# Kernel tuning notes

Hardware: AMD Instinct MI355X
Metric: run time of the kernel (lower is better)

## Reference

```python
import jax, jax.numpy as jnp
import numpy as np

N_NODES = 50000


def sage_conv(x, src, dst, W_l, b_l, W_r, n_nodes):
    """PyG SAGEConv with mean aggregation: lin_l(mean_{j->i} x_j) + lin_r(x_i)."""
    msg = x[src]                                            # [E, d]
    agg = jax.ops.segment_sum(msg, dst, num_segments=n_nodes)
    cnt = jax.ops.segment_sum(jnp.ones((src.shape[0],), x.dtype), dst,
                              num_segments=n_nodes)
    agg = agg / jnp.maximum(cnt, 1.0)[:, None]              # mean over in-neighbors
    return agg @ W_l.T + b_l + x @ W_r.T


def setup_inputs() -> dict:
    key = jax.random.key(0)
    ks = jax.random.split(key, 8)
    d_in, d_hid, d_out = 128, 128, 64
    E = 600000
    x = jax.random.normal(ks[0], (N_NODES, d_in), dtype=jnp.float32)
    edge_index = jax.random.randint(ks[1], (2, E), 0, N_NODES, dtype=jnp.int64)
    s = 1.0 / np.sqrt(d_in)
    return {
        "x": x,
        "edge_index": edge_index,
        "W1_l": jax.random.normal(ks[2], (d_hid, d_in), jnp.float32) * s,
        "b1": jnp.zeros((d_hid,), jnp.float32),
        "W1_r": jax.random.normal(ks[3], (d_hid, d_in), jnp.float32) * s,
        "W2_l": jax.random.normal(ks[4], (d_out, d_hid), jnp.float32) * s,
        "b2": jnp.zeros((d_out,), jnp.float32),
        "W2_r": jax.random.normal(ks[5], (d_out, d_hid), jnp.float32) * s,
    }


def reference(x, edge_index, W1_l, b1, W1_r, W2_l, b2, W2_r):
    src, dst = edge_index[0], edge_index[1]
    h = sage_conv(x, src, dst, W1_l, b1, W1_r, N_NODES)
    h = jax.nn.relu(h)
    h = sage_conv(h, src, dst, W2_l, b2, W2_r, N_NODES)
    return jax.nn.log_softmax(h, axis=1)
```

## Files before the change

kernel.cpp:

```cpp
#include <hip/hip_runtime.h>
#include <math.h>

#define N_NODES 50000
#define D 128
#define D_OUT 64

typedef short bf16x8 __attribute__((ext_vector_type(8)));
typedef float f32x4  __attribute__((ext_vector_type(4)));
typedef unsigned short u16x8 __attribute__((ext_vector_type(8)));

__device__ __forceinline__ unsigned short f_to_bf16(float f) {
    unsigned int u = __float_as_uint(f);
    u = (u + 0x7fffu + ((u >> 16) & 1u)) >> 16;
    return (unsigned short)u;
}
__device__ __forceinline__ float bf16lo(unsigned int v) { return __uint_as_float(v << 16); }
__device__ __forceinline__ float bf16hi(unsigned int v) { return __uint_as_float(v & 0xffff0000u); }
__device__ __forceinline__ float bf16f(unsigned short v) { return __uint_as_float((unsigned int)v << 16); }

__device__ __forceinline__ void conv8(const float* __restrict__ src, unsigned short* __restrict__ dst, int i)
{
    float4 v0 = *reinterpret_cast<const float4*>(src + i);
    float4 v1 = *reinterpret_cast<const float4*>(src + i + 4);
    u16x8 o;
    o[0] = f_to_bf16(v0.x); o[1] = f_to_bf16(v0.y);
    o[2] = f_to_bf16(v0.z); o[3] = f_to_bf16(v0.w);
    o[4] = f_to_bf16(v1.x); o[5] = f_to_bf16(v1.y);
    o[6] = f_to_bf16(v1.z); o[7] = f_to_bf16(v1.w);
    *reinterpret_cast<u16x8*>(dst + i) = o;
}

__device__ __forceinline__ void acc_add(float* acc, uint4 v)
{
    acc[0] += bf16lo(v.x); acc[1] += bf16hi(v.x);
    acc[2] += bf16lo(v.y); acc[3] += bf16hi(v.y);
    acc[4] += bf16lo(v.z); acc[5] += bf16hi(v.z);
    acc[6] += bf16lo(v.w); acc[7] += bf16hi(v.w);
}

__global__ __launch_bounds__(256) void zero_kernel(int* __restrict__ p, int n4)
{
    int i = blockIdx.x * 256 + threadIdx.x;
    if (i < n4) *reinterpret_cast<int4*>(p + i * 4) = make_int4(0, 0, 0, 0);
}

__global__ __launch_bounds__(256) void prep_kernel(
    const float* __restrict__ x, unsigned short* __restrict__ xb,
    const float* __restrict__ w1l, const float* __restrict__ w1r,
    const float* __restrict__ w2l, const float* __restrict__ w2r,
    unsigned short* __restrict__ Wb,
    const int* __restrict__ dst, int* __restrict__ deg,
    int XB, int E)
{
    const int bx = blockIdx.x;
    if (bx < XB) {
        int i = (bx * 256 + threadIdx.x) * 8;
        if (i < N_NODES * D) conv8(x, xb, i);
    } else if (bx < XB + 24) {
        int i = ((bx - XB) * 256 + threadIdx.x) * 8;
        const float* src; int off;
        if      (i < 16384) { src = w1l; off = 0; }
        else if (i < 32768) { src = w1r; off = 16384; }
        else if (i < 40960) { src = w2l; off = 32768; }
        else                { src = w2r; off = 40960; }
        conv8(src, Wb + off, i - off);
    } else {
        int e = (bx - XB - 24) * 256 + threadIdx.x;
        if (e < E) atomicAdd(&deg[dst[e]], 1);
    }
}

__global__ __launch_bounds__(256) void scan1_kernel(
    const int* __restrict__ deg, int* __restrict__ part,
    int* __restrict__ bsum, int n)
{
    const int t = threadIdx.x;
    const int base = blockIdx.x * 1024 + t * 4;

    int a0 = 0, a1 = 0, a2 = 0, a3 = 0;
    if (base + 3 < n) {
        int4 v = *reinterpret_cast<const int4*>(deg + base);
        a0 = v.x; a1 = v.y; a2 = v.z; a3 = v.w;
    } else if (base < n) {
        a0 = deg[base];
        if (base + 1 < n) a1 = deg[base + 1];
        if (base + 2 < n) a2 = deg[base + 2];
    }
    const int s0 = a0, s1 = s0 + a1, s2 = s1 + a2, s3 = s2 + a3;

    const int lane = t & 63;
    int incl = s3;
#pragma unroll
    for (int off = 1; off < 64; off <<= 1) {
        int up = __shfl_up(incl, off);
        if (lane >= off) incl += up;
    }

    __shared__ int wsum[4];
    const int wid = t >> 6;
    if (lane == 63) wsum[wid] = incl;
    __syncthreads();

    int woff = 0;
#pragma unroll
    for (int w = 0; w < 4; ++w) woff += (w < wid) ? wsum[w] : 0;

    const int ex = woff + incl - s3;
    if (base + 3 < n) {
        int4 o; o.x = ex; o.y = ex + s0; o.z = ex + s1; o.w = ex + s2;
        *reinterpret_cast<int4*>(part + base) = o;
    } else if (base < n) {
        part[base] = ex;
        if (base + 1 < n) part[base + 1] = ex + s0;
        if (base + 2 < n) part[base + 2] = ex + s1;
    }
    if (t == 255) bsum[blockIdx.x] = woff + incl;
}

__global__ __launch_bounds__(64) void scan2_kernel(
    int* __restrict__ bsum, int* __restrict__ row_ptr, int nb, int n)
{
    const int t = threadIdx.x;
    int v = (t < nb) ? bsum[t] : 0;
    int incl = v;
#pragma unroll
    for (int off = 1; off < 64; off <<= 1) {
        int up = __shfl_up(incl, off);
        if (t >= off) incl += up;
    }
    if (t < nb) bsum[t] = incl - v;
    if (t == 63) row_ptr[n] = incl;
}

__global__ __launch_bounds__(256) void scan3_kernel(
    const int* __restrict__ part, const int* __restrict__ bsum,
    int* __restrict__ row_ptr, int n)
{
    const int base = blockIdx.x * 1024 + threadIdx.x * 4;
    const int add = bsum[blockIdx.x];
    if (base + 3 < n) {
        int4 v = *reinterpret_cast<const int4*>(part + base);
        v.x += add; v.y += add; v.z += add; v.w += add;
        *reinterpret_cast<int4*>(row_ptr + base) = v;
    } else if (base < n) {
        row_ptr[base] = part[base] + add;
        if (base + 1 < n) row_ptr[base + 1] = part[base + 1] + add;
        if (base + 2 < n) row_ptr[base + 2] = part[base + 2] + add;
    }
}

__global__ __launch_bounds__(256) void fill_kernel(
    const int* __restrict__ src, const int* __restrict__ dst,
    const int* __restrict__ row_ptr, int* __restrict__ cursor,
    int* __restrict__ esrc, int E)
{
    int e = blockIdx.x * blockDim.x + threadIdx.x;
    if (e >= E) return;
    int d = dst[e];
    int pos = atomicAdd(&cursor[d], 1);
    esrc[row_ptr[d] + pos] = src[e];
}

template<int CHUNKS>
__global__ __launch_bounds__(256) void gather_bf16_kernel(
    const unsigned short* __restrict__ xb,
    const int* __restrict__ row_ptr,
    const int* __restrict__ esrc,
    unsigned short* __restrict__ aggb,
    int n_nodes)
{
    constexpr int RPL = 64 / CHUNKS;
    constexpr int NLOADS = 16 / RPL;
    const int wv   = threadIdx.x >> 6;
    const int lane = threadIdx.x & 63;
    const int node = blockIdx.x * 4 + wv;
    if (node >= n_nodes) return;

    const int beg = row_ptr[node];
    const int end = row_ptr[node + 1];
    const int g = lane / CHUNKS;
    const int c = lane % CHUNKS;

    const uint4* x4 = reinterpret_cast<const uint4*>(xb);

    float acc[8];
#pragma unroll
    for (int k = 0; k < 8; ++k) acc[k] = 0.f;

    for (int base = beg; base < end; base += 64) {
        const int cnt = min(end - base, 64);
        int s = (base + lane < end) ? esrc[base + lane] : 0;
        for (int i = 0; i < cnt; i += 16) {
            int pp[NLOADS];
            uint4 vv[NLOADS];
#pragma unroll
            for (int j = 0; j < NLOADS; ++j) {
                pp[j] = i + j * RPL + g;
                int sj = __shfl(s, pp[j]);
                vv[j] = x4[(size_t)sj * CHUNKS + c];
            }
#pragma unroll
            for (int j = 0; j < NLOADS; ++j)
                if (pp[j] < cnt) acc_add(acc, vv[j]);
        }
    }

#pragma unroll
    for (int k = 0; k < 8; ++k) {
#pragma unroll
        for (int off = CHUNKS; off < 64; off <<= 1)
            acc[k] += __shfl_xor(acc[k], off);
    }

    if (g == 0) {
        const float inv = (end > beg) ? 1.0f / (float)(end - beg) : 0.0f;
        uint4 o;
        o.x = (unsigned int)f_to_bf16(acc[0] * inv) | ((unsigned int)f_to_bf16(acc[1] * inv) << 16);
        o.y = (unsigned int)f_to_bf16(acc[2] * inv) | ((unsigned int)f_to_bf16(acc[3] * inv) << 16);
        o.z = (unsigned int)f_to_bf16(acc[4] * inv) | ((unsigned int)f_to_bf16(acc[5] * inv) << 16);
        o.w = (unsigned int)f_to_bf16(acc[6] * inv) | ((unsigned int)f_to_bf16(acc[7] * inv) << 16);
        reinterpret_cast<uint4*>(aggb)[(size_t)node * CHUNKS + c] = o;
    }
}

__global__ __launch_bounds__(64) void layer1_mfma_kernel(
    const unsigned short* __restrict__ aggb,
    const unsigned short* __restrict__ xb,
    const unsigned short* __restrict__ Wb,
    const float* __restrict__ b1,
    unsigned short* __restrict__ h1b,
    unsigned short* __restrict__ t2b)
{
    __shared__ unsigned short h1s[16][144];

    const int lane  = threadIdx.x;
    const int node0 = blockIdx.x * 16;
    const int c16   = lane & 15;
    const int kg    = lane >> 4;

    bf16x8 a[2][4];
    {
        const unsigned short* A0 = aggb + (size_t)(node0 + c16) * D + kg * 8;
        const unsigned short* A1 = xb   + (size_t)(node0 + c16) * D + kg * 8;
#pragma unroll
        for (int kf = 0; kf < 4; ++kf) {
            a[0][kf] = *reinterpret_cast<const bf16x8*>(A0 + kf * 32);
            a[1][kf] = *reinterpret_cast<const bf16x8*>(A1 + kf * 32);
        }
    }
    const unsigned short* WL = Wb;
    const unsigned short* WR = Wb + 16384;

#pragma unroll 2
    for (int jt = 0; jt < 8; ++jt) {
        f32x4 acc = {0.f, 0.f, 0.f, 0.f};
        const unsigned short* wl = WL + (size_t)(jt * 16 + c16) * D + kg * 8;
        const unsigned short* wr = WR + (size_t)(jt * 16 + c16) * D + kg * 8;
#pragma unroll
        for (int kf = 0; kf < 4; ++kf) {
            bf16x8 b = *reinterpret_cast<const bf16x8*>(wl + kf * 32);
            acc = __builtin_amdgcn_mfma_f32_16x16x32_bf16(a[0][kf], b, acc, 0, 0, 0);
        }
#pragma unroll
        for (int kf = 0; kf < 4; ++kf) {
            bf16x8 b = *reinterpret_cast<const bf16x8*>(wr + kf * 32);
            acc = __builtin_amdgcn_mfma_f32_16x16x32_bf16(a[1][kf], b, acc, 0, 0, 0);
        }
        const float bias = b1[jt * 16 + c16];
#pragma unroll
        for (int i = 0; i < 4; ++i) {
            float v = fmaxf(acc[i] + bias, 0.0f);
            unsigned short us = f_to_bf16(v);
            h1b[(size_t)(node0 + kg * 4 + i) * D + jt * 16 + c16] = us;
            h1s[kg * 4 + i][jt * 16 + c16] = us;
        }
    }

    __syncthreads();

    bf16x8 a2[4];
#pragma unroll
    for (int kf = 0; kf < 4; ++kf)
        a2[kf] = *reinterpret_cast<const bf16x8*>(&h1s[c16][kg * 8 + kf * 32]);

    const unsigned short* W2L = Wb + 32768;
#pragma unroll
    for (int jt = 0; jt < 4; ++jt) {
        f32x4 acc = {0.f, 0.f, 0.f, 0.f};
        const unsigned short* wl = W2L + (size_t)(jt * 16 + c16) * D + kg * 8;
#pragma unroll
        for (int kf = 0; kf < 4; ++kf) {
            bf16x8 b = *reinterpret_cast<const bf16x8*>(wl + kf * 32);
            acc = __builtin_amdgcn_mfma_f32_16x16x32_bf16(a2[kf], b, acc, 0, 0, 0);
        }
#pragma unroll
        for (int i = 0; i < 4; ++i)
            t2b[(size_t)(node0 + kg * 4 + i) * D_OUT + jt * 16 + c16] = f_to_bf16(acc[i]);
    }
}

__global__ __launch_bounds__(64) void layer2_mfma_kernel(
    const unsigned short* __restrict__ agg2b,
    const unsigned short* __restrict__ h1b,
    const unsigned short* __restrict__ Wb,
    const float* __restrict__ b2,
    float* __restrict__ out)
{
    const int lane  = threadIdx.x;
    const int node0 = blockIdx.x * 16;
    const int c16   = lane & 15;
    const int kg    = lane >> 4;

    bf16x8 a[4];
    {
        const unsigned short* A1 = h1b + (size_t)(node0 + c16) * D + kg * 8;
#pragma unroll
        for (int kf = 0; kf < 4; ++kf)
            a[kf] = *reinterpret_cast<const bf16x8*>(A1 + kf * 32);
    }
    const unsigned short* WR = Wb + 40960;

    f32x4 accs[4];
#pragma unroll
    for (int jt = 0; jt < 4; ++jt) {
        f32x4 acc = {0.f, 0.f, 0.f, 0.f};
        const unsigned short* wr = WR + (size_t)(jt * 16 + c16) * D + kg * 8;
#pragma unroll
        for (int kf = 0; kf < 4; ++kf) {
            bf16x8 b = *reinterpret_cast<const bf16x8*>(wr + kf * 32);
            acc = __builtin_amdgcn_mfma_f32_16x16x32_bf16(a[kf], b, acc, 0, 0, 0);
        }
        accs[jt] = acc;
    }

    float bias[4];
#pragma unroll
    for (int jt = 0; jt < 4; ++jt) bias[jt] = b2[jt * 16 + c16];

#pragma unroll
    for (int i = 0; i < 4; ++i) {
        const int node = node0 + kg * 4 + i;
        float z[4];
        float m = -1e30f;
#pragma unroll
        for (int jt = 0; jt < 4; ++jt) {
            float lft = bf16f(agg2b[(size_t)node * D_OUT + jt * 16 + c16]);
            z[jt] = lft + accs[jt][i] + bias[jt];
            m = fmaxf(m, z[jt]);
        }
#pragma unroll
        for (int off = 1; off < 16; off <<= 1)
            m = fmaxf(m, __shfl_xor(m, off));
        float s = 0.f;
#pragma unroll
        for (int jt = 0; jt < 4; ++jt) s += expf(z[jt] - m);
#pragma unroll
        for (int off = 1; off < 16; off <<= 1)
            s += __shfl_xor(s, off);
        float lse = m + logf(s);
#pragma unroll
        for (int jt = 0; jt < 4; ++jt)
            out[(size_t)node * D_OUT + jt * 16 + c16] = z[jt] - lse;
    }
}

extern "C" void kernel_launch(void* const* d_in, const int* in_sizes, int n_in,
                              void* d_out, int out_size, void* d_ws, size_t ws_size,
                              hipStream_t stream)
{
    const float* x   = (const float*)d_in[0];
    const int*   ei  = (const int*)d_in[1];
    const float* W1l = (const float*)d_in[2];
    const float* b1  = (const float*)d_in[3];
    const float* W1r = (const float*)d_in[4];
    const float* W2l = (const float*)d_in[5];
    const float* b2  = (const float*)d_in[6];
    const float* W2r = (const float*)d_in[7];
    float* out = (float*)d_out;

    const int E = in_sizes[1] / 2;
    const int* src = ei;
    const int* dst = ei + E;

    char* base = (char*)d_ws;
    size_t off = 0;
    auto take = [&](size_t bytes) { char* p = base + off; off += (bytes + 255) & ~(size_t)255; return p; };

    unsigned short* xb    = (unsigned short*)take((size_t)N_NODES * D * 2);
    unsigned short* aggb  = (unsigned short*)take((size_t)N_NODES * D * 2);
    unsigned short* h1b   = (unsigned short*)take((size_t)N_NODES * D * 2);
    unsigned short* t2b   = (unsigned short*)take((size_t)N_NODES * D_OUT * 2);
    unsigned short* agg2b = (unsigned short*)take((size_t)N_NODES * D_OUT * 2);
    unsigned short* Wb    = (unsigned short*)take((size_t)49152 * 2);
    int* degcur  = (int*)take((size_t)2 * N_NODES * 4);
    int* deg     = degcur;
    int* cursor  = degcur + N_NODES;
    int* row_ptr = (int*)take(((size_t)N_NODES + 1) * 4);
    int* part    = (int*)take((size_t)N_NODES * 4);
    int* bsum    = (int*)take((size_t)64 * 4);
    int* esrc    = (int*)take((size_t)E * 4);

    const int EB = (E + 255) / 256;
    const int SB = (N_NODES + 1023) / 1024;
    const int XB = (N_NODES * D / 8 + 255) / 256;

    zero_kernel<<<(2 * N_NODES / 4 + 255) / 256, 256, 0, stream>>>(degcur, 2 * N_NODES / 4);
    prep_kernel<<<XB + 24 + EB, 256, 0, stream>>>(x, xb, W1l, W1r, W2l, W2r, Wb, dst, deg, XB, E);
    scan1_kernel<<<SB, 256, 0, stream>>>(deg, part, bsum, N_NODES);
    scan2_kernel<<<1, 64, 0, stream>>>(bsum, row_ptr, SB, N_NODES);
    scan3_kernel<<<SB, 256, 0, stream>>>(part, bsum, row_ptr, N_NODES);
    fill_kernel<<<EB, 256, 0, stream>>>(src, dst, row_ptr, cursor, esrc, E);

    const int GB = (N_NODES + 3) / 4;
    const int MB = N_NODES / 16;

    gather_bf16_kernel<16><<<GB, 256, 0, stream>>>(xb, row_ptr, esrc, aggb, N_NODES);
    layer1_mfma_kernel<<<MB, 64, 0, stream>>>(aggb, xb, Wb, b1, h1b, t2b);

    gather_bf16_kernel<8><<<GB, 256, 0, stream>>>(t2b, row_ptr, esrc, agg2b, N_NODES);
    layer2_mfma_kernel<<<MB, 64, 0, stream>>>(agg2b, h1b, Wb, b2, out);
}
```

Baseline: 167.1 us.

## Fuse CSR build into persistent kernel and fuse gathers with MFMA layers

The degree count, three-stage scan and fill are merged into one persistent 512-block kernel that uses software grid barriers. Each gather is fused with its dense MFMA layer, so the aggregated rows stay in shared memory instead of round-tripping through global buffers. The launch count drops from ten to four. Risks: the grid barrier can deadlock if not all 512 blocks are co-resident, and the fused gather kernels run with fewer waves per node block, which may reduce memory-level parallelism during the gathers.

New measurement: 285.2 us. +70.6%, slower.

```diff
diff --git a/kernel.cpp b/kernel.cpp
--- a/kernel.cpp
+++ b/kernel.cpp
@@ -4,6 +4,7 @@
 #define N_NODES 50000
 #define D 128
 #define D_OUT 64
+#define CSRB 512
 
 typedef short bf16x8 __attribute__((ext_vector_type(8)));
 typedef float f32x4  __attribute__((ext_vector_type(4)));
@@ -38,19 +39,13 @@
     acc[6] += bf16lo(v.w); acc[7] += bf16hi(v.w);
 }
 
-__global__ __launch_bounds__(256) void zero_kernel(int* __restrict__ p, int n4)
-{
-    int i = blockIdx.x * 256 + threadIdx.x;
-    if (i < n4) *reinterpret_cast<int4*>(p + i * 4) = make_int4(0, 0, 0, 0);
-}
-
-__global__ __launch_bounds__(256) void prep_kernel(
+__global__ __launch_bounds__(256) void conv_kernel(
     const float* __restrict__ x, unsigned short* __restrict__ xb,
     const float* __restrict__ w1l, const float* __restrict__ w1r,
     const float* __restrict__ w2l, const float* __restrict__ w2r,
     unsigned short* __restrict__ Wb,
-    const int* __restrict__ dst, int* __restrict__ deg,
-    int XB, int E)
+    int* __restrict__ degcur, int* __restrict__ bar,
+    int XB, int ZB)
 {
     const int bx = blockIdx.x;
     if (bx < XB) {
@@ -64,207 +59,200 @@
         else if (i < 40960) { src = w2l; off = 32768; }
         else                { src = w2r; off = 40960; }
         conv8(src, Wb + off, i - off);
+    } else if (bx < XB + 24 + ZB) {
+        int i = (bx - XB - 24) * 256 + threadIdx.x;
+        if (i < 2 * N_NODES / 4)
+            *reinterpret_cast<int4*>(degcur + i * 4) = make_int4(0, 0, 0, 0);
     } else {
-        int e = (bx - XB - 24) * 256 + threadIdx.x;
-        if (e < E) atomicAdd(&deg[dst[e]], 1);
-    }
-}
-
-__global__ __launch_bounds__(256) void scan1_kernel(
-    const int* __restrict__ deg, int* __restrict__ part,
-    int* __restrict__ bsum, int n)
-{
+        if (threadIdx.x < 16) bar[threadIdx.x] = 0;
+    }
+}
+
+__device__ __forceinline__ void gbar(int* bar, int idx, int nblk)
+{
+    __syncthreads();
+    if (threadIdx.x == 0) {
+        __threadfence();
+        __hip_atomic_fetch_add(&bar[idx], 1, __ATOMIC_ACQ_REL, __HIP_MEMORY_SCOPE_AGENT);
+        while (__hip_atomic_load(&bar[idx], __ATOMIC_ACQUIRE, __HIP_MEMORY_SCOPE_AGENT) < nblk)
+            __builtin_amdgcn_s_sleep(1);
+        __threadfence();
+    }
+    __syncthreads();
+}
+
+__global__ __launch_bounds__(256, 2) void csr_kernel(
+    const int* __restrict__ src, const int* __restrict__ dst,
+    int* __restrict__ deg, int* __restrict__ cursor,
+    int* __restrict__ row_ptr, int* __restrict__ part,
+    int* __restrict__ bsum, int* __restrict__ esrc,
+    int* __restrict__ bar, int E)
+{
+    __shared__ int wsum[4];
+    __shared__ int sAdd, sTot;
     const int t = threadIdx.x;
-    const int base = blockIdx.x * 1024 + t * 4;
-
-    int a0 = 0, a1 = 0, a2 = 0, a3 = 0;
-    if (base + 3 < n) {
-        int4 v = *reinterpret_cast<const int4*>(deg + base);
-        a0 = v.x; a1 = v.y; a2 = v.z; a3 = v.w;
-    } else if (base < n) {
-        a0 = deg[base];
-        if (base + 1 < n) a1 = deg[base + 1];
-        if (base + 2 < n) a2 = deg[base + 2];
-    }
-    const int s0 = a0, s1 = s0 + a1, s2 = s1 + a2, s3 = s2 + a3;
-
-    const int lane = t & 63;
-    int incl = s3;
-#pragma unroll
-    for (int off = 1; off < 64; off <<= 1) {
-        int up = __shfl_up(incl, off);
-        if (lane >= off) incl += up;
-    }
-
-    __shared__ int wsum[4];
-    const int wid = t >> 6;
-    if (lane == 63) wsum[wid] = incl;
-    __syncthreads();
-
-    int woff = 0;
-#pragma unroll
-    for (int w = 0; w < 4; ++w) woff += (w < wid) ? wsum[w] : 0;
-
-    const int ex = woff + incl - s3;
-    if (base + 3 < n) {
-        int4 o; o.x = ex; o.y = ex + s0; o.z = ex + s1; o.w = ex + s2;
-        *reinterpret_cast<int4*>(part + base) = o;
-    } else if (base < n) {
-        part[base] = ex;
-        if (base + 1 < n) part[base + 1] = ex + s0;
-        if (base + 2 < n) part[base + 2] = ex + s1;
-    }
-    if (t == 255) bsum[blockIdx.x] = woff + incl;
-}
-
-__global__ __launch_bounds__(64) void scan2_kernel(
-    int* __restrict__ bsum, int* __restrict__ row_ptr, int nb, int n)
-{
-    const int t = threadIdx.x;
-    int v = (t < nb) ? bsum[t] : 0;
-    int incl = v;
-#pragma unroll
-    for (int off = 1; off < 64; off <<= 1) {
-        int up = __shfl_up(incl, off);
-        if (t >= off) incl += up;
-    }
-    if (t < nb) bsum[t] = incl - v;
-    if (t == 63) row_ptr[n] = incl;
-}
-
-__global__ __launch_bounds__(256) void scan3_kernel(
-    const int* __restrict__ part, const int* __restrict__ bsum,
-    int* __restrict__ row_ptr, int n)
-{
-    const int base = blockIdx.x * 1024 + threadIdx.x * 4;
-    const int add = bsum[blockIdx.x];
-    if (base + 3 < n) {
-        int4 v = *reinterpret_cast<const int4*>(part + base);
-        v.x += add; v.y += add; v.z += add; v.w += add;
-        *reinterpret_cast<int4*>(row_ptr + base) = v;
-    } else if (base < n) {
-        row_ptr[base] = part[base] + add;
-        if (base + 1 < n) row_ptr[base + 1] = part[base + 1] + add;
-        if (base + 2 < n) row_ptr[base + 2] = part[base + 2] + add;
-    }
-}
-
-__global__ __launch_bounds__(256) void fill_kernel(
-    const int* __restrict__ src, const int* __restrict__ dst,
-    const int* __restrict__ row_ptr, int* __restrict__ cursor,
-    int* __restrict__ esrc, int E)
-{
-    int e = blockIdx.x * blockDim.x + threadIdx.x;
-    if (e >= E) return;
-    int d = dst[e];
-    int pos = atomicAdd(&cursor[d], 1);
-    esrc[row_ptr[d] + pos] = src[e];
-}
-
-template<int CHUNKS>
-__global__ __launch_bounds__(256) void gather_bf16_kernel(
+    const int bid = blockIdx.x;
+
+    for (int e = bid * 256 + t; e < E; e += CSRB * 256)
+        atomicAdd(&deg[dst[e]], 1);
+    gbar(bar, 0, CSRB);
+
+    if (bid < 49) {
+        const int base = bid * 1024 + t * 4;
+        int a0 = 0, a1 = 0, a2 = 0, a3 = 0;
+        if (base + 3 < N_NODES) {
+            int4 v = *reinterpret_cast<const int4*>(deg + base);
+            a0 = v.x; a1 = v.y; a2 = v.z; a3 = v.w;
+        } else if (base < N_NODES) {
+            a0 = deg[base];
+            if (base + 1 < N_NODES) a1 = deg[base + 1];
+            if (base + 2 < N_NODES) a2 = deg[base + 2];
+        }
+        const int s0 = a0, s1 = s0 + a1, s2 = s1 + a2, s3 = s2 + a3;
+
+        const int lane = t & 63;
+        int incl = s3;
+#pragma unroll
+        for (int off = 1; off < 64; off <<= 1) {
+            int up = __shfl_up(incl, off);
+            if (lane >= off) incl += up;
+        }
+        const int wid = t >> 6;
+        if (lane == 63) wsum[wid] = incl;
+        __syncthreads();
+        int woff = 0;
+#pragma unroll
+        for (int w = 0; w < 4; ++w) woff += (w < wid) ? wsum[w] : 0;
+
+        const int ex = woff + incl - s3;
+        if (base + 3 < N_NODES) {
+            int4 o; o.x = ex; o.y = ex + s0; o.z = ex + s1; o.w = ex + s2;
+            *reinterpret_cast<int4*>(part + base) = o;
+        } else if (base < N_NODES) {
+            part[base] = ex;
+            if (base + 1 < N_NODES) part[base + 1] = ex + s0;
+            if (base + 2 < N_NODES) part[base + 2] = ex + s1;
+        }
+        if (t == 255) bsum[bid] = woff + incl;
+    }
+    gbar(bar, 1, CSRB);
+
+    if (bid < 49) {
+        if (t < 64) {
+            int v   = (t < 49) ? bsum[t] : 0;
+            int pre = (t < bid) ? v : 0;
+            int add = pre, tot = v;
+#pragma unroll
+            for (int off = 1; off < 64; off <<= 1) {
+                add += __shfl_xor(add, off);
+                tot += __shfl_xor(tot, off);
+            }
+            if (t == 0) { sAdd = add; sTot = tot; }
+        }
+        __syncthreads();
+        const int add = sAdd;
+        const int base = bid * 1024 + t * 4;
+        if (base + 3 < N_NODES) {
+            int4 v = *reinterpret_cast<const int4*>(part + base);
+            v.x += add; v.y += add; v.z += add; v.w += add;
+            *reinterpret_cast<int4*>(row_ptr + base) = v;
+        } else if (base < N_NODES) {
+            row_ptr[base] = part[base] + add;
+            if (base + 1 < N_NODES) row_ptr[base + 1] = part[base + 1] + add;
+            if (base + 2 < N_NODES) row_ptr[base + 2] = part[base + 2] + add;
+        }
+        if (bid == 48 && t == 0) row_ptr[N_NODES] = sTot;
+    }
+    gbar(bar, 2, CSRB);
+
+    for (int e = bid * 256 + t; e < E; e += CSRB * 256) {
+        int d = dst[e];
+        int pos = atomicAdd(&cursor[d], 1);
+        esrc[row_ptr[d] + pos] = src[e];
+    }
+}
+
+__global__ __launch_bounds__(256) void gather_layer1_kernel(
     const unsigned short* __restrict__ xb,
-    const int* __restrict__ row_ptr,
-    const int* __restrict__ esrc,
-    unsigned short* __restrict__ aggb,
-    int n_nodes)
-{
-    constexpr int RPL = 64 / CHUNKS;
-    constexpr int NLOADS = 16 / RPL;
-    const int wv   = threadIdx.x >> 6;
-    const int lane = threadIdx.x & 63;
-    const int node = blockIdx.x * 4 + wv;
-    if (node >= n_nodes) return;
-
-    const int beg = row_ptr[node];
-    const int end = row_ptr[node + 1];
-    const int g = lane / CHUNKS;
-    const int c = lane % CHUNKS;
-
-    const uint4* x4 = reinterpret_cast<const uint4*>(xb);
-
-    float acc[8];
-#pragma unroll
-    for (int k = 0; k < 8; ++k) acc[k] = 0.f;
-
-    for (int base = beg; base < end; base += 64) {
-        const int cnt = min(end - base, 64);
-        int s = (base + lane < end) ? esrc[base + lane] : 0;
-        for (int i = 0; i < cnt; i += 16) {
-            int pp[NLOADS];
-            uint4 vv[NLOADS];
-#pragma unroll
-            for (int j = 0; j < NLOADS; ++j) {
-                pp[j] = i + j * RPL + g;
-                int sj = __shfl(s, pp[j]);
-                vv[j] = x4[(size_t)sj * CHUNKS + c];
-            }
-#pragma unroll
-            for (int j = 0; j < NLOADS; ++j)
-                if (pp[j] < cnt) acc_add(acc, vv[j]);
-        }
-    }
-
-#pragma unroll
-    for (int k = 0; k < 8; ++k) {
-#pragma unroll
-        for (int off = CHUNKS; off < 64; off <<= 1)
-            acc[k] += __shfl_xor(acc[k], off);
-    }
-
-    if (g == 0) {
-        const float inv = (end > beg) ? 1.0f / (float)(end - beg) : 0.0f;
-        uint4 o;
-        o.x = (unsigned int)f_to_bf16(acc[0] * inv) | ((unsigned int)f_to_bf16(acc[1] * inv) << 16);
-        o.y = (unsigned int)f_to_bf16(acc[2] * inv) | ((unsigned int)f_to_bf16(acc[3] * inv) << 16);
-        o.z = (unsigned int)f_to_bf16(acc[4] * inv) | ((unsigned int)f_to_bf16(acc[5] * inv) << 16);
-        o.w = (unsigned int)f_to_bf16(acc[6] * inv) | ((unsigned int)f_to_bf16(acc[7] * inv) << 16);
-        reinterpret_cast<uint4*>(aggb)[(size_t)node * CHUNKS + c] = o;
-    }
-}
-
-__global__ __launch_bounds__(64) void layer1_mfma_kernel(
-    const unsigned short* __restrict__ aggb,
-    const unsigned short* __restrict__ xb,
+    const int* __restrict__ row_ptr, const int* __restrict__ esrc,
     const unsigned short* __restrict__ Wb,
     const float* __restrict__ b1,
-    unsigned short* __restrict__ h1b,
-    unsigned short* __restrict__ t2b)
-{
-    __shared__ unsigned short h1s[16][144];
-
-    const int lane  = threadIdx.x;
+    unsigned short* __restrict__ h1b, unsigned short* __restrict__ t2b)
+{
+    __shared__ unsigned short aggs[16][136];
+    __shared__ unsigned short h1s[16][136];
+
+    const int t = threadIdx.x;
+    const int wv = t >> 6, lane = t & 63;
     const int node0 = blockIdx.x * 16;
-    const int c16   = lane & 15;
-    const int kg    = lane >> 4;
-
-    bf16x8 a[2][4];
-    {
-        const unsigned short* A0 = aggb + (size_t)(node0 + c16) * D + kg * 8;
-        const unsigned short* A1 = xb   + (size_t)(node0 + c16) * D + kg * 8;
-#pragma unroll
-        for (int kf = 0; kf < 4; ++kf) {
-            a[0][kf] = *reinterpret_cast<const bf16x8*>(A0 + kf * 32);
-            a[1][kf] = *reinterpret_cast<const bf16x8*>(A1 + kf * 32);
-        }
-    }
-    const unsigned short* WL = Wb;
-    const unsigned short* WR = Wb + 16384;
-
-#pragma unroll 2
-    for (int jt = 0; jt < 8; ++jt) {
+    const int g = lane >> 4, c = lane & 15;
+    const uint4* x4 = reinterpret_cast<const uint4*>(xb);
+
+    for (int i4 = 0; i4 < 4; ++i4) {
+        const int ln = wv * 4 + i4;
+        const int node = node0 + ln;
+        const int beg = row_ptr[node], end = row_ptr[node + 1];
+
+        float acc[8];
+#pragma unroll
+        for (int k = 0; k < 8; ++k) acc[k] = 0.f;
+
+        for (int base = beg; base < end; base += 64) {
+            const int cnt = min(end - base, 64);
+            int s = (base + lane < end) ? esrc[base + lane] : 0;
+            for (int i = 0; i < cnt; i += 16) {
+                int pp[4]; uint4 vv[4];
+#pragma unroll
+                for (int j = 0; j < 4; ++j) {
+                    pp[j] = i + j * 4 + g;
+                    int sj = __shfl(s, pp[j]);
+                    vv[j] = x4[(size_t)sj * 16 + c];
+                }
+#pragma unroll
+                for (int j = 0; j < 4; ++j)
+                    if (pp[j] < cnt) acc_add(acc, vv[j]);
+            }
+        }
+#pragma unroll
+        for (int k = 0; k < 8; ++k) {
+            acc[k] += __shfl_xor(acc[k], 16);
+            acc[k] += __shfl_xor(acc[k], 32);
+        }
+        if (g == 0) {
+            const float inv = (end > beg) ? 1.0f / (float)(end - beg) : 0.0f;
+            uint4 o;
+            o.x = (unsigned int)f_to_bf16(acc[0] * inv) | ((unsigned int)f_to_bf16(acc[1] * inv) << 16);
+            o.y = (unsigned int)f_to_bf16(acc[2] * inv) | ((unsigned int)f_to_bf16(acc[3] * inv) << 16);
+            o.z = (unsigned int)f_to_bf16(acc[4] * inv) | ((unsigned int)f_to_bf16(acc[5] * inv) << 16);
+            o.w = (unsigned int)f_to_bf16(acc[6] * inv) | ((unsigned int)f_to_bf16(acc[7] * inv) << 16);
+            *reinterpret_cast<uint4*>(&aggs[ln][c * 8]) = o;
+        }
+    }
+    __syncthreads();
+
+    const int c16 = lane & 15, kg = lane >> 4;
+    bf16x8 aL[4], aR[4];
+#pragma unroll
+    for (int kf = 0; kf < 4; ++kf) {
+        aL[kf] = *reinterpret_cast<const bf16x8*>(&aggs[c16][kg * 8 + kf * 32]);
+        aR[kf] = *reinterpret_cast<const bf16x8*>(xb + (size_t)(node0 + c16) * D + kg * 8 + kf * 32);
+    }
+
+#pragma unroll
+    for (int jj = 0; jj < 2; ++jj) {
+        const int jt = wv + jj * 4;
         f32x4 acc = {0.f, 0.f, 0.f, 0.f};
-        const unsigned short* wl = WL + (size_t)(jt * 16 + c16) * D + kg * 8;
-        const unsigned short* wr = WR + (size_t)(jt * 16 + c16) * D + kg * 8;
+        const unsigned short* wl = Wb +         (size_t)(jt * 16 + c16) * D + kg * 8;
+        const unsigned short* wr = Wb + 16384 + (size_t)(jt * 16 + c16) * D + kg * 8;
 #pragma unroll
         for (int kf = 0; kf < 4; ++kf) {
             bf16x8 b = *reinterpret_cast<const bf16x8*>(wl + kf * 32);
-            acc = __builtin_amdgcn_mfma_f32_16x16x32_bf16(a[0][kf], b, acc, 0, 0, 0);
+            acc = __builtin_amdgcn_mfma_f32_16x16x32_bf16(aL[kf], b, acc, 0, 0, 0);
         }
 #pragma unroll
         for (int kf = 0; kf < 4; ++kf) {
             bf16x8 b = *reinterpret_cast<const bf16x8*>(wr + kf * 32);
-            acc = __builtin_amdgcn_mfma_f32_16x16x32_bf16(a[1][kf], b, acc, 0, 0, 0);
+            acc = __builtin_amdgcn_mfma_f32_16x16x32_bf16(aR[kf], b, acc, 0, 0, 0);
         }
         const float bias = b1[jt * 16 + c16];
 #pragma unroll
@@ -275,19 +263,16 @@
             h1s[kg * 4 + i][jt * 16 + c16] = us;
         }
     }
-
-    __syncthreads();
-
-    bf16x8 a2[4];
-#pragma unroll
-    for (int kf = 0; kf < 4; ++kf)
-        a2[kf] = *reinterpret_cast<const bf16x8*>(&h1s[c16][kg * 8 + kf * 32]);
-
-    const unsigned short* W2L = Wb + 32768;
-#pragma unroll
-    for (int jt = 0; jt < 4; ++jt) {
+    __syncthreads();
+
+    {
+        const int jt = wv;
+        bf16x8 a2[4];
+#pragma unroll
+        for (int kf = 0; kf < 4; ++kf)
+            a2[kf] = *reinterpret_cast<const bf16x8*>(&h1s[c16][kg * 8 + kf * 32]);
         f32x4 acc = {0.f, 0.f, 0.f, 0.f};
-        const unsigned short* wl = W2L + (size_t)(jt * 16 + c16) * D + kg * 8;
+        const unsigned short* wl = Wb + 32768 + (size_t)(jt * 16 + c16) * D + kg * 8;
 #pragma unroll
         for (int kf = 0; kf < 4; ++kf) {
             bf16x8 b = *reinterpret_cast<const bf16x8*>(wl + kf * 32);
@@ -299,68 +284,102 @@
     }
 }
 
-__global__ __launch_bounds__(64) void layer2_mfma_kernel(
-    const unsigned short* __restrict__ agg2b,
+__global__ __launch_bounds__(256) void gather_layer2_kernel(
+    const unsigned short* __restrict__ t2b,
     const unsigned short* __restrict__ h1b,
+    const int* __restrict__ row_ptr, const int* __restrict__ esrc,
     const unsigned short* __restrict__ Wb,
-    const float* __restrict__ b2,
-    float* __restrict__ out)
-{
-    const int lane  = threadIdx.x;
+    const float* __restrict__ b2, float* __restrict__ out)
+{
+    __shared__ unsigned short agg2s[16][72];
+    __shared__ float zs[16][68];
+
+    const int t = threadIdx.x;
+    const int wv = t >> 6, lane = t & 63;
     const int node0 = blockIdx.x * 16;
-    const int c16   = lane & 15;
-    const int kg    = lane >> 4;
-
-    bf16x8 a[4];
+    const int g = lane >> 3, c = lane & 7;
+    const uint4* t4 = reinterpret_cast<const uint4*>(t2b);
+
+    for (int i4 = 0; i4 < 4; ++i4) {
+        const int ln = wv * 4 + i4;
+        const int node = node0 + ln;
+        const int beg = row_ptr[node], end = row_ptr[node + 1];
+
+        float acc[8];
+#pragma unroll
+        for (int k = 0; k < 8; ++k) acc[k] = 0.f;
+
+        for (int base = beg; base < end; base += 64) {
+            const int cnt = min(end - base, 64);
+            int s = (base + lane < end) ? esrc[base + lane] : 0;
+            for (int i = 0; i < cnt; i += 16) {
+                int pp[2]; uint4 vv[2];
+#pragma unroll
+                for (int j = 0; j < 2; ++j) {
+                    pp[j] = i + j * 8 + g;
+                    int sj = __shfl(s, pp[j]);
+                    vv[j] = t4[(size_t)sj * 8 + c];
+                }
+#pragma unroll
+                for (int j = 0; j < 2; ++j)
+                    if (pp[j] < cnt) acc_add(acc, vv[j]);
+            }
+        }
+#pragma unroll
+        for (int k = 0; k < 8; ++k) {
+            acc[k] += __shfl_xor(acc[k], 8);
+            acc[k] += __shfl_xor(acc[k], 16);
+            acc[k] += __shfl_xor(acc[k], 32);
+        }
+        if (g == 0) {
+            const float inv = (end > beg) ? 1.0f / (float)(end - beg) : 0.0f;
+            uint4 o;
+            o.x = (unsigned int)f_to_bf16(acc[0] * inv) | ((unsigned int)f_to_bf16(acc[1] * inv) << 16);
+            o.y = (unsigned int)f_to_bf16(acc[2] * inv) | ((unsigned int)f_to_bf16(acc[3] * inv) << 16);
+            o.z = (unsigned int)f_to_bf16(acc[4] * inv) | ((unsigned int)f_to_bf16(acc[5] * inv) << 16);
+            o.w = (unsigned int)f_to_bf16(acc[6] * inv) | ((unsigned int)f_to_bf16(acc[7] * inv) << 16);
+            *reinterpret_cast<uint4*>(&agg2s[ln][c * 8]) = o;
+        }
+    }
+    __syncthreads();
+
     {
-        const unsigned short* A1 = h1b + (size_t)(node0 + c16) * D + kg * 8;
+        const int c16 = lane & 15, kg = lane >> 4;
+        const int jt = wv;
+        bf16x8 a[4];
 #pragma unroll
         for (int kf = 0; kf < 4; ++kf)
-            a[kf] = *reinterpret_cast<const bf16x8*>(A1 + kf * 32);
-    }
-    const unsigned short* WR = Wb + 40960;
-
-    f32x4 accs[4];
-#pragma unroll
-    for (int jt = 0; jt < 4; ++jt) {
+            a[kf] = *reinterpret_cast<const bf16x8*>(h1b + (size_t)(node0 + c16) * D + kg * 8 + kf * 32);
         f32x4 acc = {0.f, 0.f, 0.f, 0.f};
-        const unsigned short* wr = WR + (size_t)(jt * 16 + c16) * D + kg * 8;
+        const unsigned short* wr = Wb + 40960 + (size_t)(jt * 16 + c16) * D + kg * 8;
 #pragma unroll
         for (int kf = 0; kf < 4; ++kf) {
             bf16x8 b = *reinterpret_cast<const bf16x8*>(wr + kf * 32);
             acc = __builtin_amdgcn_mfma_f32_16x16x32_bf16(a[kf], b, acc, 0, 0, 0);
         }
-        accs[jt] = acc;
-    }
-
-    float bias[4];
-#pragma unroll
-    for (int jt = 0; jt < 4; ++jt) bias[jt] = b2[jt * 16 + c16];
-
-#pragma unroll
-    for (int i = 0; i < 4; ++i) {
-        const int node = node0 + kg * 4 + i;
-        float z[4];
-        float m = -1e30f;
-#pragma unroll
-        for (int jt = 0; jt < 4; ++jt) {
-            float lft = bf16f(agg2b[(size_t)node * D_OUT + jt * 16 + c16]);
-            z[jt] = lft + accs[jt][i] + bias[jt];
-            m = fmaxf(m, z[jt]);
-        }
-#pragma unroll
-        for (int off = 1; off < 16; off <<= 1)
+        const float bias = b2[jt * 16 + c16];
+#pragma unroll
+        for (int i = 0; i < 4; ++i) {
+            const int row = kg * 4 + i;
+            float left = bf16f(agg2s[row][jt * 16 + c16]);
+            zs[row][jt * 16 + c16] = left + acc[i] + bias;
+        }
+    }
+    __syncthreads();
+
+    for (int i4 = 0; i4 < 4; ++i4) {
+        const int ln = wv * 4 + i4;
+        float z = zs[ln][lane];
+        float m = z;
+#pragma unroll
+        for (int off = 1; off < 64; off <<= 1)
             m = fmaxf(m, __shfl_xor(m, off));
-        float s = 0.f;
-#pragma unroll
-        for (int jt = 0; jt < 4; ++jt) s += expf(z[jt] - m);
-#pragma unroll
-        for (int off = 1; off < 16; off <<= 1)
+        float e = expf(z - m);
+        float s = e;
+#pragma unroll
+        for (int off = 1; off < 64; off <<= 1)
             s += __shfl_xor(s, off);
-        float lse = m + logf(s);
-#pragma unroll
-        for (int jt = 0; jt < 4; ++jt)
-            out[(size_t)node * D_OUT + jt * 16 + c16] = z[jt] - lse;
+        out[(size_t)(node0 + ln) * D_OUT + lane] = z - m - logf(s);
     }
 }
 
@@ -386,12 +405,10 @@
     size_t off = 0;
     auto take = [&](size_t bytes) { char* p = base + off; off += (bytes + 255) & ~(size_t)255; return p; };
 
-    unsigned short* xb    = (unsigned short*)take((size_t)N_NODES * D * 2);
-    unsigned short* aggb  = (unsigned short*)take((size_t)N_NODES * D * 2);
-    unsigned short* h1b   = (unsigned short*)take((size_t)N_NODES * D * 2);
-    unsigned short* t2b   = (unsigned short*)take((size_t)N_NODES * D_OUT * 2);
-    unsigned short* agg2b = (unsigned short*)take((size_t)N_NODES * D_OUT * 2);
-    unsigned short* Wb    = (unsigned short*)take((size_t)49152 * 2);
+    unsigned short* xb  = (unsigned short*)take((size_t)N_NODES * D * 2);
+    unsigned short* h1b = (unsigned short*)take((size_t)N_NODES * D * 2);
+    unsigned short* t2b = (unsigned short*)take((size_t)N_NODES * D_OUT * 2);
+    unsigned short* Wb  = (unsigned short*)take((size_t)49152 * 2);
     int* degcur  = (int*)take((size_t)2 * N_NODES * 4);
     int* deg     = degcur;
     int* cursor  = degcur + N_NODES;
@@ -399,24 +416,18 @@
     int* part    = (int*)take((size_t)N_NODES * 4);
     int* bsum    = (int*)take((size_t)64 * 4);
     int* esrc    = (int*)take((size_t)E * 4);
-
-    const int EB = (E + 255) / 256;
-    const int SB = (N_NODES + 1023) / 1024;
+    int* bar     = (int*)take((size_t)16 * 4);
+
     const int XB = (N_NODES * D / 8 + 255) / 256;
-
-    zero_kernel<<<(2 * N_NODES / 4 + 255) / 256, 256, 0, stream>>>(degcur, 2 * N_NODES / 4);
-    prep_kernel<<<XB + 24 + EB, 256, 0, stream>>>(x, xb, W1l, W1r, W2l, W2r, Wb, dst, deg, XB, E);
-    scan1_kernel<<<SB, 256, 0, stream>>>(deg, part, bsum, N_NODES);
-    scan2_kernel<<<1, 64, 0, stream>>>(bsum, row_ptr, SB, N_NODES);
-    scan3_kernel<<<SB, 256, 0, stream>>>(part, bsum, row_ptr, N_NODES);
-    fill_kernel<<<EB, 256, 0, stream>>>(src, dst, row_ptr, cursor, esrc, E);
-
-    const int GB = (N_NODES + 3) / 4;
+    const int ZB = (2 * N_NODES / 4 + 255) / 256;
     const int MB = N_NODES / 16;
 
-    gather_bf16_kernel<16><<<GB, 256, 0, stream>>>(xb, row_ptr, esrc, aggb, N_NODES);
-    layer1_mfma_kernel<<<MB, 64, 0, stream>>>(aggb, xb, Wb, b1, h1b, t2b);
-
-    gather_bf16_kernel<8><<<GB, 256, 0, stream>>>(t2b, row_ptr, esrc, agg2b, N_NODES);
-    layer2_mfma_kernel<<<MB, 64, 0, stream>>>(agg2b, h1b, Wb, b2, out);
-}
+    conv_kernel<<<XB + 24 + ZB + 1, 256, 0, stream>>>(
+        x, xb, W1l, W1r, W2l, W2r, Wb, degcur, bar, XB, ZB);
+    csr_kernel<<<CSRB, 256, 0, stream>>>(
+        src, dst, deg, cursor, row_ptr, part, bsum, esrc, bar, E);
+    gather_layer1_kernel<<<MB, 256, 0, stream>>>(
+        xb, row_ptr, esrc, Wb, b1, h1b, t2b);
+    gather_layer2_kernel<<<MB, 256, 0, stream>>>(
+        t2b, h1b, row_ptr, esrc, Wb, b2, out);
+}
```
